# Kernel optimization log

Measured on AMD Instinct MI355X. Metric: run time of the kernel, lower is better.

The kernel has to match this reference:

```python
import jax, jax.numpy as jnp
import numpy as np
import math

D_MODEL = 1024
NUM_HEADS = 16
HEAD_DIM = D_MODEL // NUM_HEADS  # 64
THETA = 10000.0
BATCH = 2
SEQ = 2048


def setup_inputs() -> dict:
    key = jax.random.key(0)
    ks = jax.random.split(key, 5)
    scale = 0.02
    return {
        "in_features": jax.random.normal(ks[0], (BATCH, SEQ, D_MODEL), jnp.float32),
        "q_proj": jax.random.normal(ks[1], (D_MODEL, D_MODEL), jnp.float32) * scale,
        "k_proj": jax.random.normal(ks[2], (D_MODEL, D_MODEL), jnp.float32) * scale,
        "v_proj": jax.random.normal(ks[3], (D_MODEL, D_MODEL), jnp.float32) * scale,
        "o_proj": jax.random.normal(ks[4], (D_MODEL, D_MODEL), jnp.float32) * scale,
        "token_positions": jnp.arange(SEQ, dtype=jnp.int32),
    }


def _rope(x, token_positions):
    # x: [b, h, s, head_dim]; interleaved even/odd rotation
    half = HEAD_DIM // 2
    inv_freq = 1.0 / (THETA ** (2.0 * jnp.arange(half, dtype=x.dtype) / HEAD_DIM))
    angle = token_positions.astype(x.dtype)[:, None] * inv_freq[None, :]  # [s, half]
    cos, sin = jnp.cos(angle), jnp.sin(angle)
    x_e, x_o = x[..., ::2], x[..., 1::2]
    r_e = x_e * cos - x_o * sin
    r_o = x_e * sin + x_o * cos
    # interleave back: [..., s, half, 2] -> [..., s, head_dim]
    return jnp.stack([r_e, r_o], axis=-1).reshape(x.shape)


def reference(in_features, q_proj, k_proj, v_proj, o_proj, token_positions):
    b, s, _ = in_features.shape
    # projections: weight layout is [d_out, d_in]
    Q = jnp.einsum('bsd,kd->bsk', in_features, q_proj)
    K = jnp.einsum('bsd,kd->bsk', in_features, k_proj)
    V = jnp.einsum('bsd,kd->bsk', in_features, v_proj)
    # split heads: [b, h, s, head_dim]
    Q = Q.reshape(b, s, NUM_HEADS, HEAD_DIM).transpose(0, 2, 1, 3)
    K = K.reshape(b, s, NUM_HEADS, HEAD_DIM).transpose(0, 2, 1, 3)
    V = V.reshape(b, s, NUM_HEADS, HEAD_DIM).transpose(0, 2, 1, 3)
    Q = _rope(Q, token_positions)
    K = _rope(K, token_positions)
    scores = jnp.einsum('bhnd,bhmd->bhnm', Q, K) / math.sqrt(HEAD_DIM)
    causal = jnp.tril(jnp.ones((s, s), dtype=bool))  # [s, s]
    scores = jnp.where(causal[None, None], scores, -jnp.inf)
    attn = jax.nn.softmax(scores, axis=-1)
    out = jnp.einsum('bhnm,bhmd->bhnd', attn, V)
    out = out.transpose(0, 2, 1, 3).reshape(b, s, D_MODEL)
    return jnp.einsum('bsv,dv->bsd', out, o_proj)
```

## Files before the change

### kernel.cpp

```cpp
#include <hip/hip_runtime.h>
#include <hip/hip_bf16.h>

#define D_MODEL 1024
#define NHEAD   16
#define HDIM    64
#define SEQQ    2048
#define NBATCH  2
#define MROWS   (NBATCH * SEQQ)

typedef unsigned short u16;
typedef __attribute__((ext_vector_type(8))) short short8;
typedef __attribute__((ext_vector_type(4))) short bf16x4;
typedef __attribute__((ext_vector_type(4))) float floatx4;

__device__ __forceinline__ u16 f2b(float f) {
    union { __hip_bfloat16 h; u16 u; } cv;
    cv.h = __float2bfloat16(f);
    return cv.u;
}
__device__ __forceinline__ float b2f(u16 u) {
    return __uint_as_float(((unsigned int)u) << 16);
}
__device__ __forceinline__ short8 load8(const u16* p) {
    return *reinterpret_cast<const short8*>(p);
}
__device__ __forceinline__ bf16x4 load4v(const u16* p) {
    return *reinterpret_cast<const bf16x4*>(p);
}
__device__ __forceinline__ unsigned pack2(float lo, float hi) {
    return ((unsigned)f2b(hi) << 16) | (unsigned)f2b(lo);
}
__device__ __forceinline__ void async_cp16(const void* g, void* l) {
    __builtin_amdgcn_global_load_lds(
        (const __attribute__((address_space(1))) void*)g,
        (__attribute__((address_space(3))) void*)l, 16, 0, 0);
}

__global__ void cvt_all(const float* __restrict__ X,
                        const float* __restrict__ w0, const float* __restrict__ w1,
                        const float* __restrict__ w2, const float* __restrict__ w3,
                        const int* __restrict__ pos,
                        u16* __restrict__ xo,
                        u16* __restrict__ o0, u16* __restrict__ o1,
                        u16* __restrict__ o2, u16* __restrict__ o3,
                        float2* __restrict__ tab) {
    const int z = blockIdx.y;
    const int i = blockIdx.x * 256 + threadIdx.x;
    if (z == 8) {
        if (i < SEQQ * 32) {
            const int j = i >> 11, s = i & (SEQQ - 1);
            const float p = (float)pos[s];
            const float inv = expf(-(float)j * (9.210340371976184f / 32.0f));
            float sn, cs;
            sincosf(p * inv, &sn, &cs);
            tab[i] = make_float2(cs, sn);
        }
        return;
    }
    const int n4 = (D_MODEL * D_MODEL) / 4;
    const float* in;
    u16* out;
    if (z < 4) { in = X + (size_t)z * n4 * 4;  out = xo + (size_t)z * n4 * 4; }
    else {
        in  = (z == 4) ? w0 : (z == 5) ? w1 : (z == 6) ? w2 : w3;
        out = (z == 4) ? o0 : (z == 5) ? o1 : (z == 6) ? o2 : o3;
    }
    int src = i;
    if (z == 4 || z == 5) {
        const int orow = i >> 8;
        const int g    = i & 255;
        const int irow = (orow & ~63) | (((orow & 31) << 1) | ((orow >> 5) & 1));
        src = irow * 256 + g;
    }
    float4 v = reinterpret_cast<const float4*>(in)[src];
    ushort4 o;
    o.x = f2b(v.x); o.y = f2b(v.y); o.z = f2b(v.z); o.w = f2b(v.w);
    reinterpret_cast<ushort4*>(out)[i] = o;
}

__global__ __launch_bounds__(256) void gemm_qkv(
    const u16* __restrict__ A,
    const u16* __restrict__ B0, const u16* __restrict__ B1, const u16* __restrict__ B2,
    u16* __restrict__ Qt, u16* __restrict__ Kt, u16* __restrict__ Vt,
    const float2* __restrict__ tab)
{
    const int K = D_MODEL;
    const int z = blockIdx.z;
    const u16* Bt = (z == 0) ? B0 : (z == 1 ? B1 : B2);

    __shared__ __attribute__((aligned(16))) u16 As[3][128 * 32];
    __shared__ __attribute__((aligned(16))) u16 Bs[3][128 * 32];

    const int tid  = threadIdx.x;
    const int w    = tid >> 6;
    const int lane = tid & 63;
    const int l15  = lane & 15;
    const int quad = lane >> 4;
    const int wm   = w >> 1, wn = w & 1;
    const int tm   = blockIdx.x * 128, tn = blockIdx.y * 128;

    floatx4 acc[4][4];
#pragma unroll
    for (int i = 0; i < 4; i++)
#pragma unroll
        for (int j = 0; j < 4; j++) {
            floatx4 zz = {0.f, 0.f, 0.f, 0.f};
            acc[i][j] = zz;
        }

    const int srow = lane >> 2;
    const int scol = (((lane & 3) ^ ((lane >> 4) & 3))) * 8;

    auto stage = [&](int buf, int k0) {
#pragma unroll
        for (int ch = w; ch < 8; ch += 4) {
            async_cp16(A  + (size_t)(tm + ch * 16 + srow) * K + k0 + scol, &As[buf][ch * 512]);
            async_cp16(Bt + (size_t)(tn + ch * 16 + srow) * K + k0 + scol, &Bs[buf][ch * 512]);
        }
    };

    stage(0, 0);
    stage(1, 32);

    const int rchunk = (quad ^ (l15 >> 2)) * 8;

    for (int kt = 0; kt < 32; ++kt) {
        if (kt < 30) asm volatile("s_waitcnt vmcnt(4)" ::: "memory");
        else         asm volatile("s_waitcnt vmcnt(0)" ::: "memory");
        __builtin_amdgcn_s_barrier();
        if (kt < 30) stage((kt + 2) % 3, (kt + 2) * 32);

        const u16* AsB = &As[kt % 3][0];
        const u16* BsB = &Bs[kt % 3][0];

        short8 af[4], bfr[4];
#pragma unroll
        for (int mi = 0; mi < 4; mi++)
            af[mi] = load8(&AsB[(wm * 64 + mi * 16 + l15) * 32 + rchunk]);
#pragma unroll
        for (int ni = 0; ni < 4; ni++)
            bfr[ni] = load8(&BsB[(wn * 64 + ni * 16 + l15) * 32 + rchunk]);
#pragma unroll
        for (int mi = 0; mi < 4; mi++)
#pragma unroll
            for (int ni = 0; ni < 4; ni++)
                acc[mi][ni] = __builtin_amdgcn_mfma_f32_16x16x32_bf16(af[mi], bfr[ni], acc[mi][ni], 0, 0, 0);
    }

    if (z == 2) {
#pragma unroll
        for (int mi = 0; mi < 4; mi++) {
            const int r0 = tm + wm * 64 + mi * 16 + quad * 4;
            const int bb = r0 >> 11, s0 = r0 & (SEQQ - 1);
#pragma unroll
            for (int ni = 0; ni < 4; ni++) {
                const int colb = tn + wn * 64 + ni * 16 + l15;
                const int d = colb & 63, hh = colb >> 6;
                ushort4 pk;
                pk.x = f2b(acc[mi][ni][0]);
                pk.y = f2b(acc[mi][ni][1]);
                pk.z = f2b(acc[mi][ni][2]);
                pk.w = f2b(acc[mi][ni][3]);
                *reinterpret_cast<ushort4*>(
                    &Vt[(((size_t)(bb * NHEAD + hh)) * HDIM + d) * SEQQ + s0]) = pk;
            }
        }
    } else {
        const float qsc = (z == 0) ? 0.18033688011112042f : 1.0f;
        u16* Outp = (z == 0) ? Qt : Kt;
        const int hh = (tn >> 6) + wn;
        float4 ta[2], tb[2];
        auto ldtab = [&](int g) {
            const int mi = g >> 1, ni = g & 1;
            const int qq = ni * 16 + l15;
            const int s0 = (tm + wm * 64 + mi * 16 + quad * 4) & (SEQQ - 1);
            ta[g & 1] = *reinterpret_cast<const float4*>(&tab[qq * SEQQ + s0]);
            tb[g & 1] = *reinterpret_cast<const float4*>(&tab[qq * SEQQ + s0 + 2]);
        };
        ldtab(0);
#pragma unroll
        for (int g = 0; g < 8; ++g) {
            if (g < 7) ldtab(g + 1);
            const int mi = g >> 1, ni = g & 1;
            const int qq = ni * 16 + l15;
            const int r0 = tm + wm * 64 + mi * 16 + quad * 4;
            const int bb = r0 >> 11, s0 = r0 & (SEQQ - 1);
            const float4 A4 = ta[g & 1], B4 = tb[g & 1];
            const float cs[4] = {A4.x, A4.z, B4.x, B4.z};
            const float sn[4] = {A4.y, A4.w, B4.y, B4.w};
#pragma unroll
            for (int rg = 0; rg < 4; rg++) {
                const float e = acc[mi][ni][rg];
                const float o = acc[mi][ni + 2][rg];
                const unsigned val =
                    (unsigned)f2b((e * cs[rg] - o * sn[rg]) * qsc) |
                    ((unsigned)f2b((e * sn[rg] + o * cs[rg]) * qsc) << 16);
                *reinterpret_cast<unsigned*>(
                    &Outp[(((size_t)(bb * NHEAD + hh)) * SEQQ + (s0 + rg)) * HDIM + 2 * qq]) = val;
            }
        }
    }
}

__global__ __launch_bounds__(256, 4) void attn_kernel(
    const u16* __restrict__ Qt, const u16* __restrict__ Kt, const u16* __restrict__ Vt,
    u16* __restrict__ Out)
{
    const int bid = blockIdx.x;
    const int xcd = bid & 7;
    const int u   = bid >> 3;
    const int col = xcd * 4 + (u & 3);
    const int m   = u >> 2;
    int qsub;
    if      (m < 8)  qsub = 31 - m;
    else if (m < 16) qsub = m - 8;
    else if (m < 24) qsub = 39 - m;
    else             qsub = m - 16;
    const int h = col & (NHEAD - 1), b = col >> 4;

    const int tid = threadIdx.x, w = tid >> 6, lane = tid & 63;
    const int l15 = lane & 15, quad = lane >> 4;
    const size_t bh = (size_t)(b * NHEAD + h);
    const u16* Qh = Qt + bh * SEQQ * HDIM;
    const u16* Kh = Kt + bh * SEQQ * HDIM;
    const u16* Vh = Vt + bh * HDIM * SEQQ;

    __shared__ __attribute__((aligned(16))) u16 Ks[2][64 * 64];
    __shared__ __attribute__((aligned(16))) u16 Vs[2][64 * 64];

    short8 ones;
#pragma unroll
    for (int i = 0; i < 8; i++) ones[i] = (short)0x3F80;

    const int rr  = lane >> 3;
    const int swz = ((lane & 7) ^ rr) * 8;
    auto stage = [&](int buf, int tt) {
        const int k0s = tt * 64;
        async_cp16(Kh + (size_t)(k0s + w * 8 + rr) * HDIM + swz,       &Ks[buf][w * 512]);
        async_cp16(Kh + (size_t)(k0s + (w + 4) * 8 + rr) * HDIM + swz, &Ks[buf][(w + 4) * 512]);
        async_cp16(Vh + (size_t)(w * 8 + rr) * SEQQ + k0s + swz,       &Vs[buf][w * 512]);
        async_cp16(Vh + (size_t)((w + 4) * 8 + rr) * SEQQ + k0s + swz, &Vs[buf][(w + 4) * 512]);
    };

    const int s7  = l15 & 7;
    const int sw1 = ((quad)     ^ s7) * 8;
    const int sw2 = ((quad + 4) ^ s7) * 8;
    const int vo0 = (((quad >> 1)    ) ^ s7) * 8 + (quad & 1) * 4;
    const int vo1 = (((quad >> 1) + 2) ^ s7) * 8 + (quad & 1) * 4;
    const int vo2 = (((quad >> 1) + 4) ^ s7) * 8 + (quad & 1) * 4;
    const int vo3 = (((quad >> 1) + 6) ^ s7) * 8 + (quad & 1) * 4;

    const int q0w   = qsub * 64 + w * 16;
    const int tmaxp = qsub;

    short8 qf[2];
#pragma unroll
    for (int kk = 0; kk < 2; kk++)
        qf[kk] = load8(&Qh[(size_t)(q0w + l15) * HDIM + kk * 32 + quad * 8]);

    floatx4 O[4];
    floatx4 l_acc = {0.f, 0.f, 0.f, 0.f};
#pragma unroll
    for (int c = 0; c < 4; c++) { floatx4 zz = {0.f, 0.f, 0.f, 0.f}; O[c] = zz; }

    stage(0, 0);

    for (int t = 0; t <= tmaxp; ++t) {
        asm volatile("s_waitcnt vmcnt(0)" ::: "memory");
        __builtin_amdgcn_s_barrier();
        if (t < tmaxp) stage((t + 1) & 1, t + 1);

        const u16* KsB = &Ks[t & 1][0];
        const u16* VsB = &Vs[t & 1][0];
        const int k0 = t * 64;

        floatx4 S[4];
        __builtin_amdgcn_s_setprio(1);
#pragma unroll
        for (int c = 0; c < 4; c++) {
            const int rowb = (c * 16 + l15) * 64;
            floatx4 zz = {0.f, 0.f, 0.f, 0.f};
            S[c] = __builtin_amdgcn_mfma_f32_16x16x32_bf16(load8(&KsB[rowb + sw1]), qf[0], zz,   0, 0, 0);
            S[c] = __builtin_amdgcn_mfma_f32_16x16x32_bf16(load8(&KsB[rowb + sw2]), qf[1], S[c], 0, 0, 0);
        }
        __builtin_amdgcn_s_setprio(0);

        if (t == tmaxp) {
            const int q = q0w + l15;
#pragma unroll
            for (int c = 0; c < 4; c++)
#pragma unroll
                for (int r = 0; r < 4; r++)
                    if (k0 + c * 16 + quad * 4 + r > q) S[c][r] = -1e30f;
        }

#pragma unroll
        for (int c = 0; c < 4; c++)
#pragma unroll
            for (int r = 0; r < 4; r++)
                S[c][r] = __builtin_amdgcn_exp2f(S[c][r]);

        union { short8 v; unsigned u[4]; } pf0, pf1;
        pf0.u[0] = pack2(S[0][0], S[0][1]);
        pf0.u[1] = pack2(S[0][2], S[0][3]);
        pf0.u[2] = pack2(S[1][0], S[1][1]);
        pf0.u[3] = pack2(S[1][2], S[1][3]);
        pf1.u[0] = pack2(S[2][0], S[2][1]);
        pf1.u[1] = pack2(S[2][2], S[2][3]);
        pf1.u[2] = pack2(S[3][0], S[3][1]);
        pf1.u[3] = pack2(S[3][2], S[3][3]);

        __builtin_amdgcn_s_setprio(1);
        l_acc = __builtin_amdgcn_mfma_f32_16x16x32_bf16(pf0.v, ones, l_acc, 0, 0, 0);
        l_acc = __builtin_amdgcn_mfma_f32_16x16x32_bf16(pf1.v, ones, l_acc, 0, 0, 0);

#pragma unroll
        for (int c2 = 0; c2 < 4; c2++) {
            const int rowb = (c2 * 16 + l15) * 64;
            bf16x4 a0 = load4v(&VsB[rowb + vo0]);
            bf16x4 a1 = load4v(&VsB[rowb + vo1]);
            bf16x4 a2 = load4v(&VsB[rowb + vo2]);
            bf16x4 a3 = load4v(&VsB[rowb + vo3]);
            short8 v0 = __builtin_shufflevector(a0, a1, 0, 1, 2, 3, 4, 5, 6, 7);
            short8 v1 = __builtin_shufflevector(a2, a3, 0, 1, 2, 3, 4, 5, 6, 7);
            O[c2] = __builtin_amdgcn_mfma_f32_16x16x32_bf16(pf0.v, v0, O[c2], 0, 0, 0);
            O[c2] = __builtin_amdgcn_mfma_f32_16x16x32_bf16(pf1.v, v1, O[c2], 0, 0, 0);
        }
        __builtin_amdgcn_s_setprio(0);
    }

    float inv_l[4];
#pragma unroll
    for (int r = 0; r < 4; r++) inv_l[r] = 1.0f / l_acc[r];

#pragma unroll
    for (int c2 = 0; c2 < 4; c2++)
#pragma unroll
        for (int r = 0; r < 4; r++) {
            const int q    = q0w + quad * 4 + r;
            const int colo = h * HDIM + c2 * 16 + l15;
            Out[(size_t)(b * SEQQ + q) * D_MODEL + colo] = f2b(O[c2][r] * inv_l[r]);
        }
}

__global__ __launch_bounds__(256) void gemm_o(
    const u16* __restrict__ A, const u16* __restrict__ Bt, float* __restrict__ C)
{
    const int K = D_MODEL, N = D_MODEL;
    __shared__ __attribute__((aligned(16))) u16 As[3][64 * 32];
    __shared__ __attribute__((aligned(16))) u16 Bs[3][64 * 32];

    const int tid  = threadIdx.x;
    const int w    = tid >> 6;
    const int lane = tid & 63;
    const int l15  = lane & 15;
    const int quad = lane >> 4;
    const int wm   = w >> 1, wn = w & 1;
    const int tm   = blockIdx.x * 64, tn = blockIdx.y * 64;

    floatx4 acc[2][2];
#pragma unroll
    for (int i = 0; i < 2; i++)
#pragma unroll
        for (int j = 0; j < 2; j++) {
            floatx4 z = {0.f, 0.f, 0.f, 0.f};
            acc[i][j] = z;
        }

    const int srow = lane >> 2;
    const int scol = (((lane & 3) ^ ((lane >> 4) & 3))) * 8;

    auto stage = [&](int buf, int k0) {
        async_cp16(A  + (size_t)(tm + w * 16 + srow) * K + k0 + scol, &As[buf][w * 512]);
        async_cp16(Bt + (size_t)(tn + w * 16 + srow) * K + k0 + scol, &Bs[buf][w * 512]);
    };

    stage(0, 0);
    stage(1, 32);

    const int rchunk = (quad ^ (l15 >> 2)) * 8;

    for (int kt = 0; kt < 32; ++kt) {
        if (kt < 30) asm volatile("s_waitcnt vmcnt(2)" ::: "memory");
        else         asm volatile("s_waitcnt vmcnt(0)" ::: "memory");
        __builtin_amdgcn_s_barrier();
        if (kt < 30) stage((kt + 2) % 3, (kt + 2) * 32);

        const u16* AsB = &As[kt % 3][0];
        const u16* BsB = &Bs[kt % 3][0];

        short8 af[2], bfr[2];
#pragma unroll
        for (int mi = 0; mi < 2; mi++)
            af[mi] = load8(&AsB[(wm * 32 + mi * 16 + l15) * 32 + rchunk]);
#pragma unroll
        for (int ni = 0; ni < 2; ni++)
            bfr[ni] = load8(&BsB[(wn * 32 + ni * 16 + l15) * 32 + rchunk]);
#pragma unroll
        for (int mi = 0; mi < 2; mi++)
#pragma unroll
            for (int ni = 0; ni < 2; ni++)
                acc[mi][ni] = __builtin_amdgcn_mfma_f32_16x16x32_bf16(af[mi], bfr[ni], acc[mi][ni], 0, 0, 0);
    }

#pragma unroll
    for (int mi = 0; mi < 2; mi++)
#pragma unroll
        for (int ni = 0; ni < 2; ni++)
#pragma unroll
            for (int rg = 0; rg < 4; rg++) {
                int row = tm + wm * 32 + mi * 16 + quad * 4 + rg;
                int col = tn + wn * 32 + ni * 16 + l15;
                C[(size_t)row * N + col] = acc[mi][ni][rg];
            }
}

extern "C" void kernel_launch(void* const* d_in, const int* in_sizes, int n_in,
                              void* d_out, int out_size, void* d_ws, size_t ws_size,
                              hipStream_t stream)
{
    const float* X  = (const float*)d_in[0];
    const float* Wq = (const float*)d_in[1];
    const float* Wk = (const float*)d_in[2];
    const float* Wv = (const float*)d_in[3];
    const float* Wo = (const float*)d_in[4];
    const int* tpos = (const int*)d_in[5];
    float* out = (float*)d_out;
    char* ws = (char*)d_ws;

    const size_t MB = (size_t)1 << 20;
    u16*    Xb  = (u16*)(ws + 0);
    u16*    WqB = (u16*)(ws + 8 * MB);
    u16*    WkB = (u16*)(ws + 10 * MB);
    u16*    WvB = (u16*)(ws + 12 * MB);
    u16*    WoB = (u16*)(ws + 14 * MB);
    float2* tab = (float2*)(ws + 16 * MB);
    u16*    Qt  = (u16*)(ws + 24 * MB);
    u16*    Kt  = (u16*)(ws + 32 * MB);
    u16*    Vt  = (u16*)(ws + 40 * MB);
    u16*   AOut = (u16*)(ws + 48 * MB);

    cvt_all<<<dim3(1024, 9), 256, 0, stream>>>(X, Wq, Wk, Wv, Wo, tpos,
                                               Xb, WqB, WkB, WvB, WoB, tab);

    gemm_qkv<<<dim3(32, 8, 3), 256, 0, stream>>>(Xb, WqB, WkB, WvB,
                                                 Qt, Kt, Vt, tab);
    attn_kernel<<<dim3(1024, 1, 1), 256, 0, stream>>>(Qt, Kt, Vt, AOut);
    gemm_o<<<dim3(64, 16), 256, 0, stream>>>(AOut, WoB, out);
}
```

Baseline: 187.7 us.

## Shrink QKV GEMM tile to 64x128 with double buffering and unswizzled LDS

After: 186.1 us. No clear change (-0.8%).

```diff
diff --git a/kernel.cpp b/kernel.cpp
--- a/kernel.cpp
+++ b/kernel.cpp
@@ -78,7 +78,7 @@
     reinterpret_cast<ushort4*>(out)[i] = o;
 }
 
-__global__ __launch_bounds__(256) void gemm_qkv(
+__global__ __launch_bounds__(256, 6) void gemm_qkv(
     const u16* __restrict__ A,
     const u16* __restrict__ B0, const u16* __restrict__ B1, const u16* __restrict__ B2,
     u16* __restrict__ Qt, u16* __restrict__ Kt, u16* __restrict__ Vt,
@@ -88,8 +88,8 @@
     const int z = blockIdx.z;
     const u16* Bt = (z == 0) ? B0 : (z == 1 ? B1 : B2);
 
-    __shared__ __attribute__((aligned(16))) u16 As[3][128 * 32];
-    __shared__ __attribute__((aligned(16))) u16 Bs[3][128 * 32];
+    __shared__ __attribute__((aligned(16))) u16 As[2][64 * 32];
+    __shared__ __attribute__((aligned(16))) u16 Bs[2][128 * 32];
 
     const int tid  = threadIdx.x;
     const int w    = tid >> 6;
@@ -97,11 +97,11 @@
     const int l15  = lane & 15;
     const int quad = lane >> 4;
     const int wm   = w >> 1, wn = w & 1;
-    const int tm   = blockIdx.x * 128, tn = blockIdx.y * 128;
-
-    floatx4 acc[4][4];
-#pragma unroll
-    for (int i = 0; i < 4; i++)
+    const int tm   = blockIdx.x * 64, tn = blockIdx.y * 128;
+
+    floatx4 acc[2][4];
+#pragma unroll
+    for (int i = 0; i < 2; i++)
 #pragma unroll
         for (int j = 0; j < 4; j++) {
             floatx4 zz = {0.f, 0.f, 0.f, 0.f};
@@ -109,39 +109,37 @@
         }
 
     const int srow = lane >> 2;
-    const int scol = (((lane & 3) ^ ((lane >> 4) & 3))) * 8;
+    const int scol = (lane & 3) * 8;
 
     auto stage = [&](int buf, int k0) {
 #pragma unroll
-        for (int ch = w; ch < 8; ch += 4) {
-            async_cp16(A  + (size_t)(tm + ch * 16 + srow) * K + k0 + scol, &As[buf][ch * 512]);
-            async_cp16(Bt + (size_t)(tn + ch * 16 + srow) * K + k0 + scol, &Bs[buf][ch * 512]);
+        for (int ch = w; ch < 12; ch += 4) {
+            if (ch < 4) async_cp16(A  + (size_t)(tm + ch * 16 + srow) * K + k0 + scol,
+                                   &As[buf][ch * 512]);
+            else        async_cp16(Bt + (size_t)(tn + (ch - 4) * 16 + srow) * K + k0 + scol,
+                                   &Bs[buf][(ch - 4) * 512]);
         }
     };
 
     stage(0, 0);
-    stage(1, 32);
-
-    const int rchunk = (quad ^ (l15 >> 2)) * 8;
 
     for (int kt = 0; kt < 32; ++kt) {
-        if (kt < 30) asm volatile("s_waitcnt vmcnt(4)" ::: "memory");
-        else         asm volatile("s_waitcnt vmcnt(0)" ::: "memory");
+        asm volatile("s_waitcnt vmcnt(0)" ::: "memory");
         __builtin_amdgcn_s_barrier();
-        if (kt < 30) stage((kt + 2) % 3, (kt + 2) * 32);
-
-        const u16* AsB = &As[kt % 3][0];
-        const u16* BsB = &Bs[kt % 3][0];
-
-        short8 af[4], bfr[4];
-#pragma unroll
-        for (int mi = 0; mi < 4; mi++)
-            af[mi] = load8(&AsB[(wm * 64 + mi * 16 + l15) * 32 + rchunk]);
+        if (kt < 31) stage((kt + 1) & 1, (kt + 1) * 32);
+
+        const u16* AsB = &As[kt & 1][0];
+        const u16* BsB = &Bs[kt & 1][0];
+
+        short8 af[2], bfr[4];
+#pragma unroll
+        for (int mi = 0; mi < 2; mi++)
+            af[mi] = load8(&AsB[(wm * 32 + mi * 16 + l15) * 32 + quad * 8]);
 #pragma unroll
         for (int ni = 0; ni < 4; ni++)
-            bfr[ni] = load8(&BsB[(wn * 64 + ni * 16 + l15) * 32 + rchunk]);
-#pragma unroll
-        for (int mi = 0; mi < 4; mi++)
+            bfr[ni] = load8(&BsB[(wn * 64 + ni * 16 + l15) * 32 + quad * 8]);
+#pragma unroll
+        for (int mi = 0; mi < 2; mi++)
 #pragma unroll
             for (int ni = 0; ni < 4; ni++)
                 acc[mi][ni] = __builtin_amdgcn_mfma_f32_16x16x32_bf16(af[mi], bfr[ni], acc[mi][ni], 0, 0, 0);
@@ -149,8 +147,8 @@
 
     if (z == 2) {
 #pragma unroll
-        for (int mi = 0; mi < 4; mi++) {
-            const int r0 = tm + wm * 64 + mi * 16 + quad * 4;
+        for (int mi = 0; mi < 2; mi++) {
+            const int r0 = tm + wm * 32 + mi * 16 + quad * 4;
             const int bb = r0 >> 11, s0 = r0 & (SEQQ - 1);
 #pragma unroll
             for (int ni = 0; ni < 4; ni++) {
@@ -173,17 +171,17 @@
         auto ldtab = [&](int g) {
             const int mi = g >> 1, ni = g & 1;
             const int qq = ni * 16 + l15;
-            const int s0 = (tm + wm * 64 + mi * 16 + quad * 4) & (SEQQ - 1);
+            const int s0 = (tm + wm * 32 + mi * 16 + quad * 4) & (SEQQ - 1);
             ta[g & 1] = *reinterpret_cast<const float4*>(&tab[qq * SEQQ + s0]);
             tb[g & 1] = *reinterpret_cast<const float4*>(&tab[qq * SEQQ + s0 + 2]);
         };
         ldtab(0);
 #pragma unroll
-        for (int g = 0; g < 8; ++g) {
-            if (g < 7) ldtab(g + 1);
+        for (int g = 0; g < 4; ++g) {
+            if (g < 3) ldtab(g + 1);
             const int mi = g >> 1, ni = g & 1;
             const int qq = ni * 16 + l15;
-            const int r0 = tm + wm * 64 + mi * 16 + quad * 4;
+            const int r0 = tm + wm * 32 + mi * 16 + quad * 4;
             const int bb = r0 >> 11, s0 = r0 & (SEQQ - 1);
             const float4 A4 = ta[g & 1], B4 = tb[g & 1];
             const float cs[4] = {A4.x, A4.z, B4.x, B4.z};
@@ -368,7 +366,7 @@
         }
 
     const int srow = lane >> 2;
-    const int scol = (((lane & 3) ^ ((lane >> 4) & 3))) * 8;
+    const int scol = (lane & 3) * 8;
 
     auto stage = [&](int buf, int k0) {
         async_cp16(A  + (size_t)(tm + w * 16 + srow) * K + k0 + scol, &As[buf][w * 512]);
@@ -377,8 +375,6 @@
 
     stage(0, 0);
     stage(1, 32);
-
-    const int rchunk = (quad ^ (l15 >> 2)) * 8;
 
     for (int kt = 0; kt < 32; ++kt) {
         if (kt < 30) asm volatile("s_waitcnt vmcnt(2)" ::: "memory");
@@ -392,10 +388,10 @@
         short8 af[2], bfr[2];
 #pragma unroll
         for (int mi = 0; mi < 2; mi++)
-            af[mi] = load8(&AsB[(wm * 32 + mi * 16 + l15) * 32 + rchunk]);
+            af[mi] = load8(&AsB[(wm * 32 + mi * 16 + l15) * 32 + quad * 8]);
 #pragma unroll
         for (int ni = 0; ni < 2; ni++)
-            bfr[ni] = load8(&BsB[(wn * 32 + ni * 16 + l15) * 32 + rchunk]);
+            bfr[ni] = load8(&BsB[(wn * 32 + ni * 16 + l15) * 32 + quad * 8]);
 #pragma unroll
         for (int mi = 0; mi < 2; mi++)
 #pragma unroll
@@ -443,7 +439,7 @@
     cvt_all<<<dim3(1024, 9), 256, 0, stream>>>(X, Wq, Wk, Wv, Wo, tpos,
                                                Xb, WqB, WkB, WvB, WoB, tab);
 
-    gemm_qkv<<<dim3(32, 8, 3), 256, 0, stream>>>(Xb, WqB, WkB, WvB,
+    gemm_qkv<<<dim3(64, 8, 3), 256, 0, stream>>>(Xb, WqB, WkB, WvB,
                                                  Qt, Kt, Vt, tab);
     attn_kernel<<<dim3(1024, 1, 1), 256, 0, stream>>>(Qt, Kt, Vt, AOut);
     gemm_o<<<dim3(64, 16), 256, 0, stream>>>(AOut, WoB, out);
```

## Fuse all stages into one cooperative persistent kernel with grid syncs

Applied to the files above, without the earlier changes.

After: 174.4 us. 1.08x faster.

```diff
diff --git a/kernel.cpp b/kernel.cpp
--- a/kernel.cpp
+++ b/kernel.cpp
@@ -1,5 +1,6 @@
 #include <hip/hip_runtime.h>
 #include <hip/hip_bf16.h>
+#include <hip/hip_cooperative_groups.h>
 
 #define D_MODEL 1024
 #define NHEAD   16
@@ -36,17 +37,15 @@
         (__attribute__((address_space(3))) void*)l, 16, 0, 0);
 }
 
-__global__ void cvt_all(const float* __restrict__ X,
-                        const float* __restrict__ w0, const float* __restrict__ w1,
-                        const float* __restrict__ w2, const float* __restrict__ w3,
-                        const int* __restrict__ pos,
-                        u16* __restrict__ xo,
-                        u16* __restrict__ o0, u16* __restrict__ o1,
-                        u16* __restrict__ o2, u16* __restrict__ o3,
-                        float2* __restrict__ tab) {
-    const int z = blockIdx.y;
-    const int i = blockIdx.x * 256 + threadIdx.x;
-    if (z == 8) {
+
+__device__ __forceinline__ void cvt_body(
+    int bx, int zz, int tid,
+    const float* X, const float* Wq, const float* Wk, const float* Wv,
+    const float* Wo, const int* pos,
+    u16* Xb, u16* WqB, u16* WkB, u16* WvB, u16* WoB, float2* tab)
+{
+    const int i = bx * 256 + tid;
+    if (zz == 8) {
         if (i < SEQQ * 32) {
             const int j = i >> 11, s = i & (SEQQ - 1);
             const float p = (float)pos[s];
@@ -59,14 +58,14 @@
     }
     const int n4 = (D_MODEL * D_MODEL) / 4;
     const float* in;
-    u16* out;
-    if (z < 4) { in = X + (size_t)z * n4 * 4;  out = xo + (size_t)z * n4 * 4; }
+    u16* outp;
+    if (zz < 4) { in = X + (size_t)zz * n4 * 4;  outp = Xb + (size_t)zz * n4 * 4; }
     else {
-        in  = (z == 4) ? w0 : (z == 5) ? w1 : (z == 6) ? w2 : w3;
-        out = (z == 4) ? o0 : (z == 5) ? o1 : (z == 6) ? o2 : o3;
+        in   = (zz == 4) ? Wq : (zz == 5) ? Wk : (zz == 6) ? Wv : Wo;
+        outp = (zz == 4) ? WqB : (zz == 5) ? WkB : (zz == 6) ? WvB : WoB;
     }
     int src = i;
-    if (z == 4 || z == 5) {
+    if (zz == 4 || zz == 5) {
         const int orow = i >> 8;
         const int g    = i & 255;
         const int irow = (orow & ~63) | (((orow & 31) << 1) | ((orow >> 5) & 1));
@@ -75,71 +74,66 @@
     float4 v = reinterpret_cast<const float4*>(in)[src];
     ushort4 o;
     o.x = f2b(v.x); o.y = f2b(v.y); o.z = f2b(v.z); o.w = f2b(v.w);
-    reinterpret_cast<ushort4*>(out)[i] = o;
-}
-
-__global__ __launch_bounds__(256) void gemm_qkv(
-    const u16* __restrict__ A,
-    const u16* __restrict__ B0, const u16* __restrict__ B1, const u16* __restrict__ B2,
-    u16* __restrict__ Qt, u16* __restrict__ Kt, u16* __restrict__ Vt,
-    const float2* __restrict__ tab)
+    reinterpret_cast<ushort4*>(outp)[i] = o;
+}
+
+__device__ __forceinline__ void qkv_body(
+    int bid, int tid, u16* smem,
+    const u16* A, const u16* B0, const u16* B1, const u16* B2,
+    u16* Qt, u16* Kt, u16* Vt, const float2* tab)
 {
     const int K = D_MODEL;
-    const int z = blockIdx.z;
+    const int z  = bid >> 8;
+    const int bx = bid & 31;
+    const int by = (bid >> 5) & 7;
     const u16* Bt = (z == 0) ? B0 : (z == 1 ? B1 : B2);
 
-    __shared__ __attribute__((aligned(16))) u16 As[3][128 * 32];
-    __shared__ __attribute__((aligned(16))) u16 Bs[3][128 * 32];
-
-    const int tid  = threadIdx.x;
     const int w    = tid >> 6;
     const int lane = tid & 63;
     const int l15  = lane & 15;
     const int quad = lane >> 4;
     const int wm   = w >> 1, wn = w & 1;
-    const int tm   = blockIdx.x * 128, tn = blockIdx.y * 128;
+    const int tm   = bx * 128, tn = by * 128;
 
     floatx4 acc[4][4];
 #pragma unroll
     for (int i = 0; i < 4; i++)
 #pragma unroll
         for (int j = 0; j < 4; j++) {
-            floatx4 zz = {0.f, 0.f, 0.f, 0.f};
-            acc[i][j] = zz;
+            floatx4 zz4 = {0.f, 0.f, 0.f, 0.f};
+            acc[i][j] = zz4;
         }
 
     const int srow = lane >> 2;
-    const int scol = (((lane & 3) ^ ((lane >> 4) & 3))) * 8;
+    const int scol = (lane & 3) * 8;
 
     auto stage = [&](int buf, int k0) {
 #pragma unroll
         for (int ch = w; ch < 8; ch += 4) {
-            async_cp16(A  + (size_t)(tm + ch * 16 + srow) * K + k0 + scol, &As[buf][ch * 512]);
-            async_cp16(Bt + (size_t)(tn + ch * 16 + srow) * K + k0 + scol, &Bs[buf][ch * 512]);
+            async_cp16(A  + (size_t)(tm + ch * 16 + srow) * K + k0 + scol,
+                       smem + buf * 4096 + ch * 512);
+            async_cp16(Bt + (size_t)(tn + ch * 16 + srow) * K + k0 + scol,
+                       smem + 8192 + buf * 4096 + ch * 512);
         }
     };
 
     stage(0, 0);
-    stage(1, 32);
-
-    const int rchunk = (quad ^ (l15 >> 2)) * 8;
 
     for (int kt = 0; kt < 32; ++kt) {
-        if (kt < 30) asm volatile("s_waitcnt vmcnt(4)" ::: "memory");
-        else         asm volatile("s_waitcnt vmcnt(0)" ::: "memory");
+        asm volatile("s_waitcnt vmcnt(0)" ::: "memory");
         __builtin_amdgcn_s_barrier();
-        if (kt < 30) stage((kt + 2) % 3, (kt + 2) * 32);
-
-        const u16* AsB = &As[kt % 3][0];
-        const u16* BsB = &Bs[kt % 3][0];
+        if (kt < 31) stage((kt + 1) & 1, (kt + 1) * 32);
+
+        const u16* AsB = smem + (kt & 1) * 4096;
+        const u16* BsB = smem + 8192 + (kt & 1) * 4096;
 
         short8 af[4], bfr[4];
 #pragma unroll
         for (int mi = 0; mi < 4; mi++)
-            af[mi] = load8(&AsB[(wm * 64 + mi * 16 + l15) * 32 + rchunk]);
+            af[mi] = load8(&AsB[(wm * 64 + mi * 16 + l15) * 32 + quad * 8]);
 #pragma unroll
         for (int ni = 0; ni < 4; ni++)
-            bfr[ni] = load8(&BsB[(wn * 64 + ni * 16 + l15) * 32 + rchunk]);
+            bfr[ni] = load8(&BsB[(wn * 64 + ni * 16 + l15) * 32 + quad * 8]);
 #pragma unroll
         for (int mi = 0; mi < 4; mi++)
 #pragma unroll
@@ -202,11 +196,10 @@
     }
 }
 
-__global__ __launch_bounds__(256, 4) void attn_kernel(
-    const u16* __restrict__ Qt, const u16* __restrict__ Kt, const u16* __restrict__ Vt,
-    u16* __restrict__ Out)
-{
-    const int bid = blockIdx.x;
+__device__ __forceinline__ void attn_body(
+    int bid, int tid, u16* smem,
+    const u16* Qt, const u16* Kt, const u16* Vt, u16* Out)
+{
     const int xcd = bid & 7;
     const int u   = bid >> 3;
     const int col = xcd * 4 + (u & 3);
@@ -218,16 +211,13 @@
     else             qsub = m - 16;
     const int h = col & (NHEAD - 1), b = col >> 4;
 
-    const int tid = threadIdx.x, w = tid >> 6, lane = tid & 63;
+    const int w = tid >> 6, lane = tid & 63;
     const int l15 = lane & 15, quad = lane >> 4;
     const size_t bh = (size_t)(b * NHEAD + h);
     const u16* Qh = Qt + bh * SEQQ * HDIM;
     const u16* Kh = Kt + bh * SEQQ * HDIM;
     const u16* Vh = Vt + bh * HDIM * SEQQ;
 
-    __shared__ __attribute__((aligned(16))) u16 Ks[2][64 * 64];
-    __shared__ __attribute__((aligned(16))) u16 Vs[2][64 * 64];
-
     short8 ones;
 #pragma unroll
     for (int i = 0; i < 8; i++) ones[i] = (short)0x3F80;
@@ -236,10 +226,10 @@
     const int swz = ((lane & 7) ^ rr) * 8;
     auto stage = [&](int buf, int tt) {
         const int k0s = tt * 64;
-        async_cp16(Kh + (size_t)(k0s + w * 8 + rr) * HDIM + swz,       &Ks[buf][w * 512]);
-        async_cp16(Kh + (size_t)(k0s + (w + 4) * 8 + rr) * HDIM + swz, &Ks[buf][(w + 4) * 512]);
-        async_cp16(Vh + (size_t)(w * 8 + rr) * SEQQ + k0s + swz,       &Vs[buf][w * 512]);
-        async_cp16(Vh + (size_t)((w + 4) * 8 + rr) * SEQQ + k0s + swz, &Vs[buf][(w + 4) * 512]);
+        async_cp16(Kh + (size_t)(k0s + w * 8 + rr) * HDIM + swz,       smem + buf * 4096 + w * 512);
+        async_cp16(Kh + (size_t)(k0s + (w + 4) * 8 + rr) * HDIM + swz, smem + buf * 4096 + (w + 4) * 512);
+        async_cp16(Vh + (size_t)(w * 8 + rr) * SEQQ + k0s + swz,       smem + 8192 + buf * 4096 + w * 512);
+        async_cp16(Vh + (size_t)((w + 4) * 8 + rr) * SEQQ + k0s + swz, smem + 8192 + buf * 4096 + (w + 4) * 512);
     };
 
     const int s7  = l15 & 7;
@@ -261,7 +251,7 @@
     floatx4 O[4];
     floatx4 l_acc = {0.f, 0.f, 0.f, 0.f};
 #pragma unroll
-    for (int c = 0; c < 4; c++) { floatx4 zz = {0.f, 0.f, 0.f, 0.f}; O[c] = zz; }
+    for (int c = 0; c < 4; c++) { floatx4 zz4 = {0.f, 0.f, 0.f, 0.f}; O[c] = zz4; }
 
     stage(0, 0);
 
@@ -270,8 +260,8 @@
         __builtin_amdgcn_s_barrier();
         if (t < tmaxp) stage((t + 1) & 1, t + 1);
 
-        const u16* KsB = &Ks[t & 1][0];
-        const u16* VsB = &Vs[t & 1][0];
+        const u16* KsB = smem + (t & 1) * 4096;
+        const u16* VsB = smem + 8192 + (t & 1) * 4096;
         const int k0 = t * 64;
 
         floatx4 S[4];
@@ -279,8 +269,8 @@
 #pragma unroll
         for (int c = 0; c < 4; c++) {
             const int rowb = (c * 16 + l15) * 64;
-            floatx4 zz = {0.f, 0.f, 0.f, 0.f};
-            S[c] = __builtin_amdgcn_mfma_f32_16x16x32_bf16(load8(&KsB[rowb + sw1]), qf[0], zz,   0, 0, 0);
+            floatx4 zz4 = {0.f, 0.f, 0.f, 0.f};
+            S[c] = __builtin_amdgcn_mfma_f32_16x16x32_bf16(load8(&KsB[rowb + sw1]), qf[0], zz4, 0, 0, 0);
             S[c] = __builtin_amdgcn_mfma_f32_16x16x32_bf16(load8(&KsB[rowb + sw2]), qf[1], S[c], 0, 0, 0);
         }
         __builtin_amdgcn_s_setprio(0);
@@ -300,15 +290,15 @@
             for (int r = 0; r < 4; r++)
                 S[c][r] = __builtin_amdgcn_exp2f(S[c][r]);
 
-        union { short8 v; unsigned u[4]; } pf0, pf1;
-        pf0.u[0] = pack2(S[0][0], S[0][1]);
-        pf0.u[1] = pack2(S[0][2], S[0][3]);
-        pf0.u[2] = pack2(S[1][0], S[1][1]);
-        pf0.u[3] = pack2(S[1][2], S[1][3]);
-        pf1.u[0] = pack2(S[2][0], S[2][1]);
-        pf1.u[1] = pack2(S[2][2], S[2][3]);
-        pf1.u[2] = pack2(S[3][0], S[3][1]);
-        pf1.u[3] = pack2(S[3][2], S[3][3]);
+        union { short8 v; unsigned u2[4]; } pf0, pf1;
+        pf0.u2[0] = pack2(S[0][0], S[0][1]);
+        pf0.u2[1] = pack2(S[0][2], S[0][3]);
+        pf0.u2[2] = pack2(S[1][0], S[1][1]);
+        pf0.u2[3] = pack2(S[1][2], S[1][3]);
+        pf1.u2[0] = pack2(S[2][0], S[2][1]);
+        pf1.u2[1] = pack2(S[2][2], S[2][3]);
+        pf1.u2[2] = pack2(S[3][0], S[3][1]);
+        pf1.u2[3] = pack2(S[3][2], S[3][3]);
 
         __builtin_amdgcn_s_setprio(1);
         l_acc = __builtin_amdgcn_mfma_f32_16x16x32_bf16(pf0.v, ones, l_acc, 0, 0, 0);
@@ -343,42 +333,38 @@
         }
 }
 
-__global__ __launch_bounds__(256) void gemm_o(
-    const u16* __restrict__ A, const u16* __restrict__ Bt, float* __restrict__ C)
+__device__ __forceinline__ void gemmo_body(
+    int bid, int tid, u16* smem,
+    const u16* A, const u16* Bt, float* C)
 {
     const int K = D_MODEL, N = D_MODEL;
-    __shared__ __attribute__((aligned(16))) u16 As[3][64 * 32];
-    __shared__ __attribute__((aligned(16))) u16 Bs[3][64 * 32];
-
-    const int tid  = threadIdx.x;
+    const int bx = bid & 63, by = bid >> 6;
     const int w    = tid >> 6;
     const int lane = tid & 63;
     const int l15  = lane & 15;
     const int quad = lane >> 4;
     const int wm   = w >> 1, wn = w & 1;
-    const int tm   = blockIdx.x * 64, tn = blockIdx.y * 64;
+    const int tm   = bx * 64, tn = by * 64;
 
     floatx4 acc[2][2];
 #pragma unroll
     for (int i = 0; i < 2; i++)
 #pragma unroll
         for (int j = 0; j < 2; j++) {
-            floatx4 z = {0.f, 0.f, 0.f, 0.f};
-            acc[i][j] = z;
+            floatx4 z4 = {0.f, 0.f, 0.f, 0.f};
+            acc[i][j] = z4;
         }
 
     const int srow = lane >> 2;
-    const int scol = (((lane & 3) ^ ((lane >> 4) & 3))) * 8;
+    const int scol = (lane & 3) * 8;
 
     auto stage = [&](int buf, int k0) {
-        async_cp16(A  + (size_t)(tm + w * 16 + srow) * K + k0 + scol, &As[buf][w * 512]);
-        async_cp16(Bt + (size_t)(tn + w * 16 + srow) * K + k0 + scol, &Bs[buf][w * 512]);
+        async_cp16(A  + (size_t)(tm + w * 16 + srow) * K + k0 + scol, smem + buf * 2048 + w * 512);
+        async_cp16(Bt + (size_t)(tn + w * 16 + srow) * K + k0 + scol, smem + 6144 + buf * 2048 + w * 512);
     };
 
     stage(0, 0);
     stage(1, 32);
-
-    const int rchunk = (quad ^ (l15 >> 2)) * 8;
 
     for (int kt = 0; kt < 32; ++kt) {
         if (kt < 30) asm volatile("s_waitcnt vmcnt(2)" ::: "memory");
@@ -386,16 +372,16 @@
         __builtin_amdgcn_s_barrier();
         if (kt < 30) stage((kt + 2) % 3, (kt + 2) * 32);
 
-        const u16* AsB = &As[kt % 3][0];
-        const u16* BsB = &Bs[kt % 3][0];
+        const u16* AsB = smem + (kt % 3) * 2048;
+        const u16* BsB = smem + 6144 + (kt % 3) * 2048;
 
         short8 af[2], bfr[2];
 #pragma unroll
         for (int mi = 0; mi < 2; mi++)
-            af[mi] = load8(&AsB[(wm * 32 + mi * 16 + l15) * 32 + rchunk]);
+            af[mi] = load8(&AsB[(wm * 32 + mi * 16 + l15) * 32 + quad * 8]);
 #pragma unroll
         for (int ni = 0; ni < 2; ni++)
-            bfr[ni] = load8(&BsB[(wn * 32 + ni * 16 + l15) * 32 + rchunk]);
+            bfr[ni] = load8(&BsB[(wn * 32 + ni * 16 + l15) * 32 + quad * 8]);
 #pragma unroll
         for (int mi = 0; mi < 2; mi++)
 #pragma unroll
@@ -410,9 +396,80 @@
 #pragma unroll
             for (int rg = 0; rg < 4; rg++) {
                 int row = tm + wm * 32 + mi * 16 + quad * 4 + rg;
-                int col = tn + wn * 32 + ni * 16 + l15;
-                C[(size_t)row * N + col] = acc[mi][ni][rg];
+                int colo = tn + wn * 32 + ni * 16 + l15;
+                C[(size_t)row * N + colo] = acc[mi][ni][rg];
             }
+}
+
+__global__ __launch_bounds__(256, 4) void mega(
+    const float* __restrict__ X,  const float* __restrict__ Wq,
+    const float* __restrict__ Wk, const float* __restrict__ Wv,
+    const float* __restrict__ Wo, const int* __restrict__ pos,
+    u16* __restrict__ Xb,  u16* __restrict__ WqB, u16* __restrict__ WkB,
+    u16* __restrict__ WvB, u16* __restrict__ WoB, float2* __restrict__ tab,
+    u16* __restrict__ Qt, u16* __restrict__ Kt, u16* __restrict__ Vt,
+    u16* __restrict__ AOut, float* __restrict__ out)
+{
+    cooperative_groups::grid_group grid = cooperative_groups::this_grid();
+    __shared__ __attribute__((aligned(16))) u16 smem[16384];
+
+    const int tid  = threadIdx.x;
+    const int bid0 = blockIdx.x;
+
+    for (int vb = bid0; vb < 9216; vb += 1024)
+        cvt_body(vb & 1023, vb >> 10, tid, X, Wq, Wk, Wv, Wo, pos,
+                 Xb, WqB, WkB, WvB, WoB, tab);
+    __threadfence();
+    grid.sync();
+
+    if (bid0 < 768)
+        qkv_body(bid0, tid, smem, Xb, WqB, WkB, WvB, Qt, Kt, Vt, tab);
+    __threadfence();
+    grid.sync();
+
+    attn_body(bid0, tid, smem, Qt, Kt, Vt, AOut);
+    __threadfence();
+    grid.sync();
+
+    gemmo_body(bid0, tid, smem, AOut, WoB, out);
+}
+
+__global__ void cvt_all_k(const float* __restrict__ X,
+                          const float* __restrict__ w0, const float* __restrict__ w1,
+                          const float* __restrict__ w2, const float* __restrict__ w3,
+                          const int* __restrict__ pos,
+                          u16* __restrict__ xo,
+                          u16* __restrict__ o0, u16* __restrict__ o1,
+                          u16* __restrict__ o2, u16* __restrict__ o3,
+                          float2* __restrict__ tab) {
+    cvt_body(blockIdx.x, blockIdx.y, threadIdx.x, X, w0, w1, w2, w3, pos,
+             xo, o0, o1, o2, o3, tab);
+}
+
+__global__ __launch_bounds__(256) void gemm_qkv_k(
+    const u16* __restrict__ A,
+    const u16* __restrict__ B0, const u16* __restrict__ B1, const u16* __restrict__ B2,
+    u16* __restrict__ Qt, u16* __restrict__ Kt, u16* __restrict__ Vt,
+    const float2* __restrict__ tab)
+{
+    __shared__ __attribute__((aligned(16))) u16 smem[16384];
+    const int bid = blockIdx.x + blockIdx.y * 32 + blockIdx.z * 256;
+    qkv_body(bid, threadIdx.x, smem, A, B0, B1, B2, Qt, Kt, Vt, tab);
+}
+
+__global__ __launch_bounds__(256, 4) void attn_k(
+    const u16* __restrict__ Qt, const u16* __restrict__ Kt, const u16* __restrict__ Vt,
+    u16* __restrict__ Out)
+{
+    __shared__ __attribute__((aligned(16))) u16 smem[16384];
+    attn_body(blockIdx.x, threadIdx.x, smem, Qt, Kt, Vt, Out);
+}
+
+__global__ __launch_bounds__(256) void gemm_o_k(
+    const u16* __restrict__ A, const u16* __restrict__ Bt, float* __restrict__ C)
+{
+    __shared__ __attribute__((aligned(16))) u16 smem[12288];
+    gemmo_body(blockIdx.x + blockIdx.y * 64, threadIdx.x, smem, A, Bt, C);
 }
 
 extern "C" void kernel_launch(void* const* d_in, const int* in_sizes, int n_in,
@@ -440,11 +497,31 @@
     u16*    Vt  = (u16*)(ws + 40 * MB);
     u16*   AOut = (u16*)(ws + 48 * MB);
 
-    cvt_all<<<dim3(1024, 9), 256, 0, stream>>>(X, Wq, Wk, Wv, Wo, tpos,
-                                               Xb, WqB, WkB, WvB, WoB, tab);
-
-    gemm_qkv<<<dim3(32, 8, 3), 256, 0, stream>>>(Xb, WqB, WkB, WvB,
-                                                 Qt, Kt, Vt, tab);
-    attn_kernel<<<dim3(1024, 1, 1), 256, 0, stream>>>(Qt, Kt, Vt, AOut);
-    gemm_o<<<dim3(64, 16), 256, 0, stream>>>(AOut, WoB, out);
-}
+    static int use_coop = -1;
+    if (use_coop < 0) {
+        int nb = 0;
+        hipError_t e = hipOccupancyMaxActiveBlocksPerMultiprocessor(
+            &nb, reinterpret_cast<const void*>(&mega), 256, 0);
+        int dev = 0, coop = 0;
+        hipGetDevice(&dev);
+        hipDeviceGetAttribute(&coop, hipDeviceAttributeCooperativeLaunch, dev);
+        use_coop = (e == hipSuccess && nb >= 4 && coop) ? 1 : 0;
+    }
+
+    if (use_coop) {
+        void* args[] = {
+            (void*)&X, (void*)&Wq, (void*)&Wk, (void*)&Wv, (void*)&Wo, (void*)&tpos,
+            (void*)&Xb, (void*)&WqB, (void*)&WkB, (void*)&WvB, (void*)&WoB, (void*)&tab,
+            (void*)&Qt, (void*)&Kt, (void*)&Vt, (void*)&AOut, (void*)&out
+        };
+        hipLaunchCooperativeKernel(reinterpret_cast<const void*>(&mega),
+                                   dim3(1024), dim3(256), args, 0, stream);
+    } else {
+        cvt_all_k<<<dim3(1024, 9), 256, 0, stream>>>(X, Wq, Wk, Wv, Wo, tpos,
+                                                     Xb, WqB, WkB, WvB, WoB, tab);
+        gemm_qkv_k<<<dim3(32, 8, 3), 256, 0, stream>>>(Xb, WqB, WkB, WvB,
+                                                       Qt, Kt, Vt, tab);
+        attn_k<<<dim3(1024, 1, 1), 256, 0, stream>>>(Qt, Kt, Vt, AOut);
+        gemm_o_k<<<dim3(64, 16), 256, 0, stream>>>(AOut, WoB, out);
+    }
+}
```
